# Optimization experiments

Measured on AMD Instinct MI355X. Metric: run time of the kernel, lower is better.

The kernel has to match this reference:

```python
import jax, jax.numpy as jnp
import numpy as np

H = 512      # hidden_size
GH = 512     # global_hidden_size
V = 128      # VOCAB_SIZE (one-hot arg_hot width)
D = 14       # tree depth; complete binary tree
NUM_OPS = 36
N_INT = 5    # num_internal_ops
N_NODES = 2 ** (D + 1) - 1  # 32767, heap layout: node i has children 2i+1, 2i+2


def _p(key, i, shape, s=0.05):
    return jax.random.normal(jax.random.fold_in(key, i), shape, dtype=jnp.float32) * s


def setup_inputs() -> dict:
    key = jax.random.key(0)
    return {
        "tokens": jax.random.randint(jax.random.fold_in(key, 0), (N_NODES,), 0, V),
        "validity_mask": jnp.ones((NUM_OPS,), jnp.float32),
        # binary tree-LSTM (blstm): 2 children
        "W_iou_b": _p(key, 1, (V, 3 * H)), "U_iou_b": _p(key, 2, (2, H, 3 * H)), "b_iou_b": jnp.zeros((3 * H,), jnp.float32),
        "Wf_b": _p(key, 3, (V, H)), "Uf_b": _p(key, 4, (2, H, H)), "bf_b": jnp.ones((H,), jnp.float32),
        # ternary tree-LSTM (tlstm): 3 children
        "W_iou_t": _p(key, 5, (V, 3 * H)), "U_iou_t": _p(key, 6, (3, H, 3 * H)), "b_iou_t": jnp.zeros((3 * H,), jnp.float32),
        "Wf_t": _p(key, 7, (V, H)), "Uf_t": _p(key, 8, (3, H, H)), "bf_t": jnp.ones((H,), jnp.float32),
        # FFN: one h-by-h layer (ffn_complexity = h^2 * n_layers, n_layers=1)
        "ffn_W": _p(key, 9, (H, H)), "ffn_b": jnp.zeros((H,), jnp.float32),
        # global LSTM (1 layer, 1 step), torch gate order i,f,g,o
        "lstm_Wx": _p(key, 10, (H, 4 * GH)), "lstm_Wh": _p(key, 11, (GH, 4 * GH)), "lstm_b": jnp.zeros((4 * GH,), jnp.float32),
        # actor heads on concat(root_hidden, h_glob)
        "hl_W": _p(key, 12, (H + GH, 2)), "hl_b": jnp.zeros((2,), jnp.float32),
        "int_W": _p(key, 13, (H + GH, N_INT)), "int_b": jnp.zeros((N_INT,), jnp.float32),
        "act_W": _p(key, 14, (H + GH, NUM_OPS)), "act_b": jnp.zeros((NUM_OPS,), jnp.float32),
    }


def _nary_cell(x, hk, ck, W_iou, U_iou, b_iou, Wf, Uf, bf):
    # x: [n, V]; hk, ck: [n, K, H]  (K children)
    iou = x @ W_iou + jnp.einsum('nkh,khg->ng', hk, U_iou) + b_iou
    i, o, u = jnp.split(iou, 3, axis=-1)
    f = jax.nn.sigmoid((x @ Wf + bf)[:, None, :] + jnp.einsum('nkh,khg->nkg', hk, Uf))
    c = jax.nn.sigmoid(i) * jnp.tanh(u) + jnp.sum(f * ck, axis=1)
    h = jax.nn.sigmoid(o) * jnp.tanh(c)
    return h, c


def _forward(tokens, validity_mask, W_iou_b, U_iou_b, b_iou_b, Wf_b, Uf_b, bf_b,
             W_iou_t, U_iou_t, b_iou_t, Wf_t, Uf_t, bf_t, ffn_W, ffn_b,
             lstm_Wx, lstm_Wh, lstm_b, hl_W, hl_b, int_W, int_b, act_W, act_b):
    arg_hot = jax.nn.one_hot(tokens, V, dtype=jnp.float32)  # [N_NODES, V]
    h_prev = c_prev = None
    h_ab = c_ab = None
    # apply_binary_lstm over the whole tree, bottom-up, one batched cell per level
    for lvl in range(D, -1, -1):
        n = 2 ** lvl
        x = arg_hot[n - 1:2 * n - 1]  # level lvl occupies heap slots [2^l-1, 2^{l+1}-2]
        if h_prev is None:
            hk = jnp.zeros((n, 2, H), jnp.float32)  # leaves: tz children
            ck = hk
        else:
            hk = h_prev.reshape(n, 2, H)
            ck = c_prev.reshape(n, 2, H)
        h_prev, c_prev = _nary_cell(x, hk, ck, W_iou_b, U_iou_b, b_iou_b, Wf_b, Uf_b, bf_b)
        if lvl == 1:
            h_ab, c_ab = h_prev, c_prev  # root's children a, b
    # apply_ternary_lstm at depth 0: children = (self.hidden, a.hidden, b.hidden)
    hk3 = jnp.concatenate([h_prev, h_ab], axis=0)[None]  # [1, 3, H]
    ck3 = jnp.concatenate([c_prev, c_ab], axis=0)[None]
    h_root, c_root = _nary_cell(arg_hot[0:1], hk3, ck3, W_iou_t, U_iou_t, b_iou_t, Wf_t, Uf_t, bf_t)
    # apply_ffn (1 layer) then apply_global_lstm (single step from zero state)
    h_f = jnp.maximum(h_root @ ffn_W + ffn_b, 0.0)  # [1, H]
    h_g = jnp.zeros((1, GH), jnp.float32)
    c_g = h_g
    gates = h_f @ lstm_Wx + h_g @ lstm_Wh + lstm_b
    gi, gf, gg, go = jnp.split(gates, 4, axis=-1)
    c_g = jax.nn.sigmoid(gf) * c_g + jax.nn.sigmoid(gi) * jnp.tanh(gg)
    h_g = jax.nn.sigmoid(go) * jnp.tanh(c_g)
    # actor heads
    feat = jnp.concatenate([h_f, h_g], axis=-1)  # [1, H+GH]
    hl = feat @ hl_W + hl_b
    il = feat @ int_W + int_b
    el = jnp.log(validity_mask)[None, :] + feat @ (act_W * validity_mask[None, :]) + act_b * validity_mask
    return jnp.concatenate([hl, il, el], axis=-1)  # [1, 2 + N_INT + NUM_OPS]


def reference(tokens, validity_mask, W_iou_b, U_iou_b, b_iou_b, Wf_b, Uf_b, bf_b,
              W_iou_t, U_iou_t, b_iou_t, Wf_t, Uf_t, bf_t, ffn_W, ffn_b,
              lstm_Wx, lstm_Wh, lstm_b, hl_W, hl_b, int_W, int_b, act_W, act_b):
    return _forward(tokens, validity_mask, W_iou_b, U_iou_b, b_iou_b, Wf_b, Uf_b, bf_b,
                    W_iou_t, U_iou_t, b_iou_t, Wf_t, Uf_t, bf_t, ffn_W, ffn_b,
                    lstm_Wx, lstm_Wh, lstm_b, hl_W, hl_b, int_W, int_b, act_W, act_b)
```

## Files before the change

kernel.cpp:

```cpp
#include <hip/hip_runtime.h>
#include <hip/hip_bf16.h>
#include <math.h>

#define H 512
#define V 128
#define NLEAF 16384

typedef __attribute__((ext_vector_type(4))) float f32x4;
typedef __attribute__((ext_vector_type(8))) short s16x8;
typedef __attribute__((ext_vector_type(4))) unsigned short u16x4;
typedef unsigned short ushort_t;

__device__ ushort_t g_hb0[NLEAF * H];
__device__ ushort_t g_hb1[(NLEAF / 2) * H];
__device__ float    g_c0[NLEAF * H];
__device__ float    g_c1[(NLEAF / 2) * H];
__device__ ushort_t g_UiouT[3 * H * 2 * H];
__device__ ushort_t g_UfT[H * 2 * H];
__device__ ushort_t g_UiouTt[3 * H * 3 * H];
__device__ ushort_t g_UfTt[H * 3 * H];
__device__ float    g_rpart[3 * 3072];
__device__ float    g_root[2 * H];
__device__ float    g_hf[H];
__device__ float    g_gates[4 * H];

__device__ __forceinline__ float sigm(float x) { return 1.0f / (1.0f + __expf(-x)); }
__device__ __forceinline__ float ftanh(float x) {
  return 1.0f - 2.0f / (__expf(2.0f * x) + 1.0f);
}
__device__ __forceinline__ ushort_t f2bf(float x) {
  __hip_bfloat16 b = __float2bfloat16(x);
  return *reinterpret_cast<ushort_t*>(&b);
}
__device__ __forceinline__ float bf2f(ushort_t u) {
  union { unsigned int i; float f; } v; v.i = ((unsigned int)u) << 16; return v.f;
}
__device__ __forceinline__ void gload_lds16(const void* g, void* l) {
  __builtin_amdgcn_global_load_lds(
      (const __attribute__((address_space(1))) unsigned int*)g,
      (__attribute__((address_space(3))) unsigned int*)l, 16, 0, 0);
}

__global__ __launch_bounds__(256) void k_transp_all(
    const float* __restrict__ s0, const float* __restrict__ s1,
    const float* __restrict__ s2, const float* __restrict__ s3,
    ushort_t* __restrict__ d0, ushort_t* __restrict__ d1,
    ushort_t* __restrict__ d2, ushort_t* __restrict__ d3) {
  const float* src; ushort_t* dst; int R, Cc;
  switch (blockIdx.z) {
    case 0: src = s0; dst = d0; R = 1024; Cc = 1536; break;
    case 1: src = s1; dst = d1; R = 1024; Cc = 512; break;
    case 2: src = s2; dst = d2; R = 1536; Cc = 1536; break;
    default: src = s3; dst = d3; R = 1536; Cc = 512; break;
  }
  int bc = blockIdx.x * 32, br = blockIdx.y * 32;
  if (bc >= Cc || br >= R) return;
  __shared__ float t[32][33];
  int tx = threadIdx.x & 31, ty = threadIdx.x >> 5;
  for (int rr = ty; rr < 32; rr += 8)
    t[rr][tx] = src[(size_t)(br + rr) * Cc + bc + tx];
  __syncthreads();
  for (int rr = ty; rr < 32; rr += 8)
    dst[(size_t)(bc + rr) * R + br + tx] = f2bf(t[tx][rr]);
}

__global__ __launch_bounds__(256) void k_leaf(const int* __restrict__ tokens,
                                              const float* __restrict__ Wiou,
                                              const float* __restrict__ biou) {
  const int total = NLEAF * 128;
  for (int q = blockIdx.x * 256 + threadIdx.x; q < total; q += gridDim.x * 256) {
    int i = q >> 7, jv = q & 127;
    int tok = tokens[(NLEAF - 1) + i];
    const f32x4* Wr = (const f32x4*)(Wiou + (size_t)tok * 1536);
    const f32x4* bv = (const f32x4*)biou;
    f32x4 wi = Wr[jv] + bv[jv];
    f32x4 wo = Wr[128 + jv] + bv[128 + jv];
    f32x4 wu = Wr[256 + jv] + bv[256 + jv];
    u16x4 hv; f32x4 cv;
    #pragma unroll
    for (int r = 0; r < 4; ++r) {
      float c = sigm(wi[r]) * ftanh(wu[r]);
      float h = sigm(wo[r]) * ftanh(c);
      cv[r] = c;
      hv[r] = f2bf(h);
    }
    *reinterpret_cast<u16x4*>(&g_hb0[(size_t)q * 4]) = hv;
    *reinterpret_cast<f32x4*>(&g_c0[(size_t)q * 4]) = cv;
  }
}

__global__ __launch_bounds__(256, 2) void k_mfma_lvl(int lvl,
    const int* __restrict__ tokens,
    const float* __restrict__ Wiou, const float* __restrict__ biou,
    const float* __restrict__ Wf, const float* __restrict__ bf) {
  const int n = 1 << lvl;
  const int node0 = n - 1;
  const int outp = lvl & 1;
  const ushort_t* __restrict__ hprev = outp ? g_hb0 : g_hb1;
  const float* __restrict__ cprev = outp ? g_c0 : g_c1;
  ushort_t* __restrict__ hout = outp ? g_hb1 : g_hb0;
  float* __restrict__ cout = outp ? g_c1 : g_c0;

  const int i0 = blockIdx.x * 128;
  const int j0 = blockIdx.y * 64;
  const int tid = threadIdx.x;
  const int lane = tid & 63;
  const int w = tid >> 6;
  const int wry = w >> 1;
  const int cx = w & 1;

  __shared__ f32x4 smemv[3072];
  char* smem = (char*)smemv;

  const char* gp[6];
  unsigned lb[6], lstride[6];
  {
    int kb = (lane >> 4) * 16;
    #pragma unroll
    for (int q = 0; q < 6; ++q) {
      int c = w * 6 + q;
      if (c < 8) {
        int row = i0 + c * 16 + (lane & 15);
        gp[q] = (const char*)hprev + (size_t)row * 2048 + kb;
        lb[q] = c * 1024u;
        lstride[q] = 8192u;
      } else {
        int ct = c - 8;
        int col = ct * 16 + (lane & 15);
        int g = col >> 6, jj = j0 + (col & 63);
        const ushort_t* Ub = (g < 3) ? (g_UiouT + (size_t)(g * 512 + jj) * 1024)
                                     : (g_UfT + (size_t)jj * 1024);
        gp[q] = (const char*)Ub + kb;
        lb[q] = 16384u + ct * 1024u;
        lstride[q] = 16384u;
      }
    }
  }

#define STAGE(BUF)                                                   \
  {                                                                  \
    _Pragma("unroll")                                                \
    for (int q = 0; q < 6; ++q) {                                    \
      gload_lds16(gp[q], smem + lb[q] + (unsigned)(BUF) * lstride[q]); \
      gp[q] += 64;                                                   \
    }                                                                \
  }

  f32x4 acc[4][10];
  #pragma unroll
  for (int a = 0; a < 4; ++a)
    #pragma unroll
    for (int b = 0; b < 10; ++b) acc[a][b] = (f32x4){0.f, 0.f, 0.f, 0.f};

#define COMPUTE(FA)                                                          \
  {                                                                          \
    const char* ab = smem + buf * 8192 + wry * 4096 + lane * 16;             \
    s16x8 a0 = *(const s16x8*)(ab);                                          \
    s16x8 a1 = *(const s16x8*)(ab + 1024);                                   \
    s16x8 a2 = *(const s16x8*)(ab + 2048);                                   \
    s16x8 a3 = *(const s16x8*)(ab + 3072);                                   \
    const char* bb = smem + 16384 + buf * 16384 + cx * 2048 + lane * 16;     \
    s16x8 b0 = *(const s16x8*)(bb);                                          \
    s16x8 b1 = *(const s16x8*)(bb + 1024);                                   \
    s16x8 b2 = *(const s16x8*)(bb + 4096);                                   \
    s16x8 b3 = *(const s16x8*)(bb + 5120);                                   \
    s16x8 b4 = *(const s16x8*)(bb + 8192);                                   \
    s16x8 b5 = *(const s16x8*)(bb + 9216);                                   \
    s16x8 b6 = *(const s16x8*)(bb + 12288);                                  \
    s16x8 b7 = *(const s16x8*)(bb + 13312);                                  \
    s16x8 aa[4] = {a0, a1, a2, a3};                                          \
    _Pragma("unroll")                                                        \
    for (int rtl = 0; rtl < 4; ++rtl) {                                      \
      acc[rtl][0] = __builtin_amdgcn_mfma_f32_16x16x32_bf16(aa[rtl], b0, acc[rtl][0], 0, 0, 0); \
      acc[rtl][1] = __builtin_amdgcn_mfma_f32_16x16x32_bf16(aa[rtl], b1, acc[rtl][1], 0, 0, 0); \
      acc[rtl][2] = __builtin_amdgcn_mfma_f32_16x16x32_bf16(aa[rtl], b2, acc[rtl][2], 0, 0, 0); \
      acc[rtl][3] = __builtin_amdgcn_mfma_f32_16x16x32_bf16(aa[rtl], b3, acc[rtl][3], 0, 0, 0); \
      acc[rtl][4] = __builtin_amdgcn_mfma_f32_16x16x32_bf16(aa[rtl], b4, acc[rtl][4], 0, 0, 0); \
      acc[rtl][5] = __builtin_amdgcn_mfma_f32_16x16x32_bf16(aa[rtl], b5, acc[rtl][5], 0, 0, 0); \
      acc[rtl][FA] = __builtin_amdgcn_mfma_f32_16x16x32_bf16(aa[rtl], b6, acc[rtl][FA], 0, 0, 0); \
      acc[rtl][FA + 1] = __builtin_amdgcn_mfma_f32_16x16x32_bf16(aa[rtl], b7, acc[rtl][FA + 1], 0, 0, 0); \
    }                                                                        \
  }

  STAGE(0);
  __syncthreads();
  int buf = 0;
  for (int kt = 0; kt < 16; ++kt) {
    STAGE(buf ^ 1);
    COMPUTE(6);
    __syncthreads();
    buf ^= 1;
  }
  for (int kt = 16; kt < 32; ++kt) {
    if (kt < 31) STAGE(buf ^ 1);
    COMPUTE(8);
    __syncthreads();
    buf ^= 1;
  }
#undef COMPUTE
#undef STAGE

  const int node_c = lane >> 4;
  const int jl = lane & 15;
  #pragma unroll
  for (int t = 0; t < 2; ++t) {
    const int j = j0 + cx * 32 + t * 16 + jl;
    const float bi = biou[j], bo = biou[512 + j], bu = biou[1024 + j], bfv = bf[j];
    #pragma unroll
    for (int rtl = 0; rtl < 4; ++rtl) {
      f32x4 vi = acc[rtl][0 + t], vo = acc[rtl][2 + t], vu = acc[rtl][4 + t],
            v0 = acc[rtl][6 + t], v1 = acc[rtl][8 + t];
      const int ib = i0 + wry * 64 + rtl * 16 + node_c * 4;
      #pragma unroll
      for (int r = 0; r < 4; ++r) {
        int i = ib + r;
        int tok = tokens[node0 + i];
        const float* Wr = Wiou + (size_t)tok * 1536;
        float fpre = Wf[(size_t)tok * 512 + j] + bfv;
        float ig = vi[r] + Wr[j] + bi;
        float og = vo[r] + Wr[512 + j] + bo;
        float ug = vu[r] + Wr[1024 + j] + bu;
        float cc = sigm(ig) * ftanh(ug)
                 + sigm(fpre + v0[r]) * cprev[(size_t)(2 * i) * 512 + j]
                 + sigm(fpre + v1[r]) * cprev[(size_t)(2 * i + 1) * 512 + j];
        float hh = sigm(og) * ftanh(cc);
        hout[(size_t)i * 512 + j] = f2bf(hh);
        cout[(size_t)i * 512 + j] = cc;
      }
    }
  }
}

__global__ __launch_bounds__(256) void k_small(int lvl,
    const int* __restrict__ tokens,
    const float* __restrict__ Wiou, const float* __restrict__ biou,
    const float* __restrict__ Wf, const float* __restrict__ bf) {
  const int n = 1 << lvl;
  const int node0 = n - 1;
  const int outp = lvl & 1;
  const ushort_t* __restrict__ hprev = outp ? g_hb0 : g_hb1;
  const float* __restrict__ cprev = outp ? g_c0 : g_c1;
  ushort_t* __restrict__ hout = outp ? g_hb1 : g_hb0;
  float* __restrict__ cout = outp ? g_c1 : g_c0;

  const int i = blockIdx.y;
  const int j0 = blockIdx.x * 64;
  const int tid = threadIdx.x;
  const int g = tid >> 6;
  const int jc = tid & 63;
  const int jj = j0 + jc;

  __shared__ float hl[1024];
  __shared__ float exch[5][64];
  for (int t = tid; t < 1024; t += 256) hl[t] = bf2f(hprev[(size_t)i * 1024 + t]);
  __syncthreads();

  const ushort_t* col = (g < 3) ? (g_UiouT + (size_t)(g * 512 + jj) * 1024)
                                : (g_UfT + (size_t)jj * 1024);
  float a0 = 0.f, a1 = 0.f;
  #pragma unroll 4
  for (int k0 = 0; k0 < 512; k0 += 8) {
    s16x8 wv = *(const s16x8*)(col + k0);
    #pragma unroll
    for (int r = 0; r < 8; ++r) a0 += hl[k0 + r] * bf2f((ushort_t)wv[r]);
  }
  #pragma unroll 4
  for (int k0 = 512; k0 < 1024; k0 += 8) {
    s16x8 wv = *(const s16x8*)(col + k0);
    #pragma unroll
    for (int r = 0; r < 8; ++r) a1 += hl[k0 + r] * bf2f((ushort_t)wv[r]);
  }
  if (g < 3) exch[g][jc] = a0 + a1;
  else { exch[3][jc] = a0; exch[4][jc] = a1; }
  __syncthreads();

  if (tid < 64) {
    int j = j0 + tid;
    float ai = exch[0][tid], ao = exch[1][tid], au = exch[2][tid];
    float af0 = exch[3][tid], af1 = exch[4][tid];
    int tok = tokens[node0 + i];
    const float* Wr = Wiou + (size_t)tok * 1536;
    float fpre = Wf[(size_t)tok * 512 + j] + bf[j];
    float ig = ai + Wr[j] + biou[j];
    float og = ao + Wr[512 + j] + biou[512 + j];
    float ug = au + Wr[1024 + j] + biou[1024 + j];
    float cc = sigm(ig) * ftanh(ug)
             + sigm(fpre + af0) * cprev[(size_t)(2 * i) * 512 + j]
             + sigm(fpre + af1) * cprev[(size_t)(2 * i + 1) * 512 + j];
    float hh = sigm(og) * ftanh(cc);
    hout[(size_t)i * 512 + j] = f2bf(hh);
    cout[(size_t)i * 512 + j] = cc;
  }
}

__global__ __launch_bounds__(256) void k_root_p1() {
  const int by = blockIdx.y;
  const int tid = threadIdx.x;
  const int c = blockIdx.x * 256 + tid;

  __shared__ float hl[512];
  {
    int m0 = by * 512;
    #pragma unroll
    for (int q = 0; q < 2; ++q) {
      int t = tid + q * 256, m = m0 + t;
      hl[t] = (m < 512) ? bf2f(g_hb0[m]) : bf2f(g_hb1[m - 512]);
    }
  }
  __syncthreads();

  float acc = 0.f;
  const ushort_t* col = nullptr;
  if (c < 1536) {
    col = g_UiouTt + (size_t)c * 1536 + by * 512;
  } else {
    int v = c - 1536;
    if ((v >> 9) == by) col = g_UfTt + (size_t)(v & 511) * 1536 + by * 512;
  }
  if (col) {
    #pragma unroll 4
    for (int k0 = 0; k0 < 512; k0 += 8) {
      s16x8 wv = *(const s16x8*)(col + k0);
      #pragma unroll
      for (int r = 0; r < 8; ++r) acc += hl[k0 + r] * bf2f((ushort_t)wv[r]);
    }
  }
  g_rpart[(size_t)by * 3072 + c] = acc;
}

__global__ __launch_bounds__(512) void k_root_p2(const int* __restrict__ tokens,
    const float* __restrict__ Wiou_t, const float* __restrict__ biou_t,
    const float* __restrict__ Wf_t, const float* __restrict__ bf_t) {
  const int j = threadIdx.x;
  float ai = g_rpart[j] + g_rpart[3072 + j] + g_rpart[6144 + j];
  float ao = g_rpart[512 + j] + g_rpart[3072 + 512 + j] + g_rpart[6144 + 512 + j];
  float au = g_rpart[1024 + j] + g_rpart[3072 + 1024 + j] + g_rpart[6144 + 1024 + j];
  float f0 = g_rpart[1536 + j] + g_rpart[3072 + 1536 + j] + g_rpart[6144 + 1536 + j];
  float f1 = g_rpart[2048 + j] + g_rpart[3072 + 2048 + j] + g_rpart[6144 + 2048 + j];
  float f2 = g_rpart[2560 + j] + g_rpart[3072 + 2560 + j] + g_rpart[6144 + 2560 + j];

  int tok = tokens[0];
  float fpre = Wf_t[(size_t)tok * H + j] + bf_t[j];
  float ig = ai + Wiou_t[(size_t)tok * 3 * H + j] + biou_t[j];
  float og = ao + Wiou_t[(size_t)tok * 3 * H + H + j] + biou_t[H + j];
  float ug = au + Wiou_t[(size_t)tok * 3 * H + 2 * H + j] + biou_t[2 * H + j];
  float cc = sigm(ig) * ftanh(ug)
           + sigm(fpre + f0) * g_c0[j]
           + sigm(fpre + f1) * g_c1[j]
           + sigm(fpre + f2) * g_c1[H + j];
  float hh = sigm(og) * ftanh(cc);
  g_root[j] = hh;
  g_root[H + j] = cc;
}

__global__ __launch_bounds__(512) void k_head1(const float* __restrict__ ffnW,
                                               const float* __restrict__ ffnb) {
  __shared__ float hr[H];
  int j = threadIdx.x;
  hr[j] = g_root[j];
  __syncthreads();
  float acc = ffnb[j];
  #pragma unroll 8
  for (int m = 0; m < H; ++m) acc += hr[m] * ffnW[m * H + j];
  g_hf[j] = fmaxf(acc, 0.0f);
}

__global__ __launch_bounds__(64) void k_head2(const float* __restrict__ Wx,
                                              const float* __restrict__ lb) {
  int g = blockIdx.x * 64 + threadIdx.x;
  float acc = lb[g];
  #pragma unroll 8
  for (int m = 0; m < H; ++m) acc += g_hf[m] * Wx[m * 4 * H + g];
  g_gates[g] = acc;
}

__global__ __launch_bounds__(512) void k_head3(const float* __restrict__ vm,
    const float* __restrict__ hlW, const float* __restrict__ hlb,
    const float* __restrict__ intW, const float* __restrict__ intb,
    const float* __restrict__ actW, const float* __restrict__ actb,
    float* __restrict__ out) {
  __shared__ float feat[2 * H];
  int j = threadIdx.x;
  float ci = sigm(g_gates[j]) * ftanh(g_gates[2 * H + j]);
  float hg = sigm(g_gates[3 * H + j]) * ftanh(ci);
  feat[j] = g_hf[j];
  feat[H + j] = hg;
  __syncthreads();

  const int wv = threadIdx.x >> 6;
  const int lane = threadIdx.x & 63;
  for (int o = wv; o < 43; o += 8) {
    const float* Wc;
    int stride, colb;
    if (o < 2)       { Wc = hlW;  stride = 2;  colb = o; }
    else if (o < 7)  { Wc = intW; stride = 5;  colb = o - 2; }
    else             { Wc = actW; stride = 36; colb = o - 7; }
    float s = 0.f;
    #pragma unroll
    for (int q = 0; q < 16; ++q) {
      int m = lane + q * 64;
      s += feat[m] * Wc[(size_t)m * stride + colb];
    }
    #pragma unroll
    for (int d = 32; d >= 1; d >>= 1) s += __shfl_xor(s, d);
    if (lane == 0) {
      float res;
      if (o < 2)      res = s + hlb[o];
      else if (o < 7) res = s + intb[o - 2];
      else {
        int a = o - 7;
        float v = vm[a];
        res = __logf(v) + s * v + actb[a] * v;
      }
      out[o] = res;
    }
  }
}

extern "C" void kernel_launch(void* const* d_in, const int* in_sizes, int n_in,
                              void* d_out, int out_size, void* d_ws, size_t ws_size,
                              hipStream_t stream) {
  (void)in_sizes; (void)n_in; (void)d_ws; (void)ws_size; (void)out_size;
  const int* tokens   = (const int*)d_in[0];
  const float* vm     = (const float*)d_in[1];
  const float* Wiou_b = (const float*)d_in[2];
  const float* Uiou_b = (const float*)d_in[3];
  const float* biou_b = (const float*)d_in[4];
  const float* Wf_b   = (const float*)d_in[5];
  const float* Uf_b   = (const float*)d_in[6];
  const float* bf_b   = (const float*)d_in[7];
  const float* Wiou_t = (const float*)d_in[8];
  const float* Uiou_t = (const float*)d_in[9];
  const float* biou_t = (const float*)d_in[10];
  const float* Wf_t   = (const float*)d_in[11];
  const float* Uf_t   = (const float*)d_in[12];
  const float* bf_t   = (const float*)d_in[13];
  const float* ffnW   = (const float*)d_in[14];
  const float* ffnb   = (const float*)d_in[15];
  const float* lstmWx = (const float*)d_in[16];
  const float* lstmb  = (const float*)d_in[18];
  const float* hlW    = (const float*)d_in[19];
  const float* hlb    = (const float*)d_in[20];
  const float* intW   = (const float*)d_in[21];
  const float* intb   = (const float*)d_in[22];
  const float* actW   = (const float*)d_in[23];
  const float* actb   = (const float*)d_in[24];

  ushort_t* UiouT;  hipGetSymbolAddress((void**)&UiouT, HIP_SYMBOL(g_UiouT));
  ushort_t* UfT;    hipGetSymbolAddress((void**)&UfT, HIP_SYMBOL(g_UfT));
  ushort_t* UiouTt; hipGetSymbolAddress((void**)&UiouTt, HIP_SYMBOL(g_UiouTt));
  ushort_t* UfTt;   hipGetSymbolAddress((void**)&UfTt, HIP_SYMBOL(g_UfTt));

  k_transp_all<<<dim3(48, 48, 4), 256, 0, stream>>>(
      Uiou_b, Uf_b, Uiou_t, Uf_t, UiouT, UfT, UiouTt, UfTt);

  k_leaf<<<2048, 256, 0, stream>>>(tokens, Wiou_b, biou_b);
  for (int lvl = 13; lvl >= 8; --lvl) {
    int gx = (1 << lvl) / 128;
    k_mfma_lvl<<<dim3(gx, 8), 256, 0, stream>>>(lvl, tokens, Wiou_b, biou_b,
                                                Wf_b, bf_b);
  }
  for (int lvl = 7; lvl >= 0; --lvl) {
    int n = 1 << lvl;
    k_small<<<dim3(8, n), 256, 0, stream>>>(lvl, tokens, Wiou_b, biou_b,
                                            Wf_b, bf_b);
  }
  k_root_p1<<<dim3(12, 3), 256, 0, stream>>>();
  k_root_p2<<<1, 512, 0, stream>>>(tokens, Wiou_t, biou_t, Wf_t, bf_t);
  k_head1<<<1, 512, 0, stream>>>(ffnW, ffnb);
  k_head2<<<32, 64, 0, stream>>>(lstmWx, lstmb);
  k_head3<<<1, 512, 0, stream>>>(vm, hlW, hlb, intW, intb, actW, actb, (float*)d_out);
}
```

Measured before the change: 658.6 us.

## Merge leaf/transpose and root/head kernels, deepen MFMA prefetch, remap blocks, skip forget-gate

Fuses the leaf-cell computation into the weight transpose launch and the root cell into the first head GEMV, removing two kernel launches. In the level MFMA kernel it issues two stages ahead with explicit vmcnt waits and raw barriers, raises wave priority around MFMA blocks, raises the occupancy hint to 3, and remaps the 1D grid so tiles sharing weight columns are spread across dispatch order. The head2 kernel stops computing the global-LSTM forget gate, which is multiplied by a zero cell state. These changes trade simpler synchronisation and lower register budget for less launch overhead and better overlap.

```diff
diff --git a/kernel.cpp b/kernel.cpp
--- a/kernel.cpp
+++ b/kernel.cpp
@@ -20,7 +20,6 @@
 __device__ ushort_t g_UiouTt[3 * H * 3 * H];
 __device__ ushort_t g_UfTt[H * 3 * H];
 __device__ float    g_rpart[3 * 3072];
-__device__ float    g_root[2 * H];
 __device__ float    g_hf[H];
 __device__ float    g_gates[4 * H];
 
@@ -41,11 +40,37 @@
       (__attribute__((address_space(3))) unsigned int*)l, 16, 0, 0);
 }
 
-__global__ __launch_bounds__(256) void k_transp_all(
+__global__ __launch_bounds__(256) void k_prep(
     const float* __restrict__ s0, const float* __restrict__ s1,
     const float* __restrict__ s2, const float* __restrict__ s3,
     ushort_t* __restrict__ d0, ushort_t* __restrict__ d1,
-    ushort_t* __restrict__ d2, ushort_t* __restrict__ d3) {
+    ushort_t* __restrict__ d2, ushort_t* __restrict__ d3,
+    const int* __restrict__ tokens,
+    const float* __restrict__ Wiou, const float* __restrict__ biou) {
+  if (blockIdx.z == 4) {
+    const int total = NLEAF * 128;
+    const int bid = blockIdx.y * 48 + blockIdx.x;
+    for (int q = bid * 256 + threadIdx.x; q < total; q += 2304 * 256) {
+      int i = q >> 7, jv = q & 127;
+      int tok = tokens[(NLEAF - 1) + i];
+      const f32x4* Wr = (const f32x4*)(Wiou + (size_t)tok * 1536);
+      const f32x4* bv = (const f32x4*)biou;
+      f32x4 wi = Wr[jv] + bv[jv];
+      f32x4 wo = Wr[128 + jv] + bv[128 + jv];
+      f32x4 wu = Wr[256 + jv] + bv[256 + jv];
+      u16x4 hv; f32x4 cv;
+      #pragma unroll
+      for (int r = 0; r < 4; ++r) {
+        float c = sigm(wi[r]) * ftanh(wu[r]);
+        float h = sigm(wo[r]) * ftanh(c);
+        cv[r] = c;
+        hv[r] = f2bf(h);
+      }
+      *reinterpret_cast<u16x4*>(&g_hb0[(size_t)q * 4]) = hv;
+      *reinterpret_cast<f32x4*>(&g_c0[(size_t)q * 4]) = cv;
+    }
+    return;
+  }
   const float* src; ushort_t* dst; int R, Cc;
   switch (blockIdx.z) {
     case 0: src = s0; dst = d0; R = 1024; Cc = 1536; break;
@@ -64,32 +89,7 @@
     dst[(size_t)(bc + rr) * R + br + tx] = f2bf(t[tx][rr]);
 }
 
-__global__ __launch_bounds__(256) void k_leaf(const int* __restrict__ tokens,
-                                              const float* __restrict__ Wiou,
-                                              const float* __restrict__ biou) {
-  const int total = NLEAF * 128;
-  for (int q = blockIdx.x * 256 + threadIdx.x; q < total; q += gridDim.x * 256) {
-    int i = q >> 7, jv = q & 127;
-    int tok = tokens[(NLEAF - 1) + i];
-    const f32x4* Wr = (const f32x4*)(Wiou + (size_t)tok * 1536);
-    const f32x4* bv = (const f32x4*)biou;
-    f32x4 wi = Wr[jv] + bv[jv];
-    f32x4 wo = Wr[128 + jv] + bv[128 + jv];
-    f32x4 wu = Wr[256 + jv] + bv[256 + jv];
-    u16x4 hv; f32x4 cv;
-    #pragma unroll
-    for (int r = 0; r < 4; ++r) {
-      float c = sigm(wi[r]) * ftanh(wu[r]);
-      float h = sigm(wo[r]) * ftanh(c);
-      cv[r] = c;
-      hv[r] = f2bf(h);
-    }
-    *reinterpret_cast<u16x4*>(&g_hb0[(size_t)q * 4]) = hv;
-    *reinterpret_cast<f32x4*>(&g_c0[(size_t)q * 4]) = cv;
-  }
-}
-
-__global__ __launch_bounds__(256, 2) void k_mfma_lvl(int lvl,
+__global__ __launch_bounds__(256, 3) void k_mfma_lvl(int lvl,
     const int* __restrict__ tokens,
     const float* __restrict__ Wiou, const float* __restrict__ biou,
     const float* __restrict__ Wf, const float* __restrict__ bf) {
@@ -101,8 +101,12 @@
   ushort_t* __restrict__ hout = outp ? g_hb1 : g_hb0;
   float* __restrict__ cout = outp ? g_c1 : g_c0;
 
-  const int i0 = blockIdx.x * 128;
-  const int j0 = blockIdx.y * 64;
+  const int orig = blockIdx.x;
+  const int qch = gridDim.x >> 3;
+  const int wg = (orig & 7) * qch + (orig >> 3);
+  const int i0 = (wg >> 3) * 128;
+  const int j0 = (wg & 7) * 64;
+
   const int tid = threadIdx.x;
   const int lane = tid & 63;
   const int w = tid >> 6;
@@ -145,6 +149,8 @@
       gp[q] += 64;                                                   \
     }                                                                \
   }
+#define WAITV(N) asm volatile("s_waitcnt vmcnt(" #N ")" ::: "memory")
+#define BAR_IN()  { __builtin_amdgcn_s_barrier(); __builtin_amdgcn_sched_barrier(0); }
 
   f32x4 acc[4][10];
   #pragma unroll
@@ -169,6 +175,7 @@
     s16x8 b6 = *(const s16x8*)(bb + 12288);                                  \
     s16x8 b7 = *(const s16x8*)(bb + 13312);                                  \
     s16x8 aa[4] = {a0, a1, a2, a3};                                          \
+    __builtin_amdgcn_s_setprio(1);                                           \
     _Pragma("unroll")                                                        \
     for (int rtl = 0; rtl < 4; ++rtl) {                                      \
       acc[rtl][0] = __builtin_amdgcn_mfma_f32_16x16x32_bf16(aa[rtl], b0, acc[rtl][0], 0, 0, 0); \
@@ -180,25 +187,33 @@
       acc[rtl][FA] = __builtin_amdgcn_mfma_f32_16x16x32_bf16(aa[rtl], b6, acc[rtl][FA], 0, 0, 0); \
       acc[rtl][FA + 1] = __builtin_amdgcn_mfma_f32_16x16x32_bf16(aa[rtl], b7, acc[rtl][FA + 1], 0, 0, 0); \
     }                                                                        \
-  }
-
-  STAGE(0);
-  __syncthreads();
+    __builtin_amdgcn_s_setprio(0);                                           \
+  }
+
+  STAGE(0); STAGE(1);
   int buf = 0;
   for (int kt = 0; kt < 16; ++kt) {
-    STAGE(buf ^ 1);
+    WAITV(6);
+    BAR_IN();
     COMPUTE(6);
-    __syncthreads();
+    BAR_IN();
+    STAGE(buf);
     buf ^= 1;
   }
-  for (int kt = 16; kt < 32; ++kt) {
-    if (kt < 31) STAGE(buf ^ 1);
+  for (int kt = 16; kt < 30; ++kt) {
+    WAITV(6);
+    BAR_IN();
     COMPUTE(8);
-    __syncthreads();
+    BAR_IN();
+    STAGE(buf);
     buf ^= 1;
   }
+  WAITV(6); BAR_IN(); COMPUTE(8); buf ^= 1;
+  WAITV(0); BAR_IN(); COMPUTE(8);
 #undef COMPUTE
 #undef STAGE
+#undef WAITV
+#undef BAR_IN
 
   const int node_c = lane >> 4;
   const int jl = lane & 15;
@@ -328,9 +343,11 @@
   g_rpart[(size_t)by * 3072 + c] = acc;
 }
 
-__global__ __launch_bounds__(512) void k_root_p2(const int* __restrict__ tokens,
+__global__ __launch_bounds__(512) void k_p2h1(const int* __restrict__ tokens,
     const float* __restrict__ Wiou_t, const float* __restrict__ biou_t,
-    const float* __restrict__ Wf_t, const float* __restrict__ bf_t) {
+    const float* __restrict__ Wf_t, const float* __restrict__ bf_t,
+    const float* __restrict__ ffnW, const float* __restrict__ ffnb) {
+  __shared__ float hroot[H];
   const int j = threadIdx.x;
   float ai = g_rpart[j] + g_rpart[3072 + j] + g_rpart[6144 + j];
   float ao = g_rpart[512 + j] + g_rpart[3072 + 512 + j] + g_rpart[6144 + 512 + j];
@@ -348,30 +365,25 @@
            + sigm(fpre + f0) * g_c0[j]
            + sigm(fpre + f1) * g_c1[j]
            + sigm(fpre + f2) * g_c1[H + j];
-  float hh = sigm(og) * ftanh(cc);
-  g_root[j] = hh;
-  g_root[H + j] = cc;
-}
-
-__global__ __launch_bounds__(512) void k_head1(const float* __restrict__ ffnW,
-                                               const float* __restrict__ ffnb) {
-  __shared__ float hr[H];
-  int j = threadIdx.x;
-  hr[j] = g_root[j];
-  __syncthreads();
+  hroot[j] = sigm(og) * ftanh(cc);
+  __syncthreads();
+
   float acc = ffnb[j];
   #pragma unroll 8
-  for (int m = 0; m < H; ++m) acc += hr[m] * ffnW[m * H + j];
+  for (int m = 0; m < H; ++m) acc += hroot[m] * ffnW[m * H + j];
   g_hf[j] = fmaxf(acc, 0.0f);
 }
 
 __global__ __launch_bounds__(64) void k_head2(const float* __restrict__ Wx,
                                               const float* __restrict__ lb) {
-  int g = blockIdx.x * 64 + threadIdx.x;
-  float acc = lb[g];
+  int idx = blockIdx.x * 64 + threadIdx.x;
+  int region = idx >> 9;
+  int j = idx & 511;
+  int g2 = (region == 0) ? j : ((region == 1) ? 1024 + j : 1536 + j);
+  float acc = lb[g2];
   #pragma unroll 8
-  for (int m = 0; m < H; ++m) acc += g_hf[m] * Wx[m * 4 * H + g];
-  g_gates[g] = acc;
+  for (int m = 0; m < H; ++m) acc += g_hf[m] * Wx[m * 4 * H + g2];
+  g_gates[g2] = acc;
 }
 
 __global__ __launch_bounds__(512) void k_head3(const float* __restrict__ vm,
@@ -451,14 +463,14 @@
   ushort_t* UiouTt; hipGetSymbolAddress((void**)&UiouTt, HIP_SYMBOL(g_UiouTt));
   ushort_t* UfTt;   hipGetSymbolAddress((void**)&UfTt, HIP_SYMBOL(g_UfTt));
 
-  k_transp_all<<<dim3(48, 48, 4), 256, 0, stream>>>(
-      Uiou_b, Uf_b, Uiou_t, Uf_t, UiouT, UfT, UiouTt, UfTt);
-
-  k_leaf<<<2048, 256, 0, stream>>>(tokens, Wiou_b, biou_b);
+  k_prep<<<dim3(48, 48, 5), 256, 0, stream>>>(
+      Uiou_b, Uf_b, Uiou_t, Uf_t, UiouT, UfT, UiouTt, UfTt,
+      tokens, Wiou_b, biou_b);
+
   for (int lvl = 13; lvl >= 8; --lvl) {
-    int gx = (1 << lvl) / 128;
-    k_mfma_lvl<<<dim3(gx, 8), 256, 0, stream>>>(lvl, tokens, Wiou_b, biou_b,
-                                                Wf_b, bf_b);
+    int nb = ((1 << lvl) / 128) * 8;
+    k_mfma_lvl<<<nb, 256, 0, stream>>>(lvl, tokens, Wiou_b, biou_b,
+                                       Wf_b, bf_b);
   }
   for (int lvl = 7; lvl >= 0; --lvl) {
     int n = 1 << lvl;
@@ -466,8 +478,7 @@
                                             Wf_b, bf_b);
   }
   k_root_p1<<<dim3(12, 3), 256, 0, stream>>>();
-  k_root_p2<<<1, 512, 0, stream>>>(tokens, Wiou_t, biou_t, Wf_t, bf_t);
-  k_head1<<<1, 512, 0, stream>>>(ffnW, ffnb);
-  k_head2<<<32, 64, 0, stream>>>(lstmWx, lstmb);
+  k_p2h1<<<1, 512, 0, stream>>>(tokens, Wiou_t, biou_t, Wf_t, bf_t, ffnW, ffnb);
+  k_head2<<<24, 64, 0, stream>>>(lstmWx, lstmb);
   k_head3<<<1, 512, 0, stream>>>(vm, hlW, hlb, intW, intb, actW, actb, (float*)d_out);
 }
```

After: 1.456 ms. +121.1%, slower.
